# Performance work log

Measured on AMD Instinct MI355X. Metric: run time of the kernel, lower is better.

Reference implementation:

```python
import jax, jax.numpy as jnp
import numpy as np

N_DATA = 32768
N_CHK = 32768
N = N_DATA + N_CHK          # 65536 nodes
E = 524288                  # edges (before self-loops)
F_IN = 10                   # node_feature_dim
HID = 128                   # hidden_dim
HEADS = 4
C = HID // HEADS            # 32 per-head channels
L = 4                       # num_gnn_layers
EPS_LN = 1e-5


def layer_norm(x, g, b):
    mu = x.mean(-1, keepdims=True)
    var = ((x - mu) ** 2).mean(-1, keepdims=True)
    return (x - mu) * jax.lax.rsqrt(var + EPS_LN) * g + b


def mlp3(x, W1, b1, W2, b2, W3, b3):
    h = jax.nn.relu(x @ W1 + b1)
    h = jax.nn.relu(h @ W2 + b2)
    return h @ W3 + b3


def setup_inputs() -> dict:
    key = jax.random.key(0)
    ks = jax.random.split(key, 32)
    s = 0.02
    inp = {
        'node_features': jax.random.normal(ks[0], (N, F_IN), jnp.float32),
        'edge_index': jax.random.randint(ks[1], (2, E), 0, N, dtype=jnp.int64),
        # node embedding: Linear(F_IN,HID) + LayerNorm
        'W_emb': s * jax.random.normal(ks[2], (F_IN, HID), jnp.float32),
        'b_emb': jnp.zeros((HID,), jnp.float32),
        'ln0_g': jnp.ones((HID,), jnp.float32),
        'ln0_b': jnp.zeros((HID,), jnp.float32),
        # L GATConv layers (stacked): lin weight, att_src/att_dst, bias, post-LN
        'Wg': s * jax.random.normal(ks[3], (L, HID, HID), jnp.float32),
        'att_s': s * jax.random.normal(ks[4], (L, HEADS, C), jnp.float32),
        'att_d': s * jax.random.normal(ks[5], (L, HEADS, C), jnp.float32),
        'bg': jnp.zeros((L, HID), jnp.float32),
        'lng': jnp.ones((L, HID), jnp.float32),
        'lnb': jnp.zeros((L, HID), jnp.float32),
        # policy net
        'pW1': s * jax.random.normal(ks[6], (HID, HID), jnp.float32),
        'pb1': jnp.zeros((HID,), jnp.float32),
        'pW2': s * jax.random.normal(ks[7], (HID, HID // 2), jnp.float32),
        'pb2': jnp.zeros((HID // 2,), jnp.float32),
        'pW3': s * jax.random.normal(ks[8], (HID // 2, 2), jnp.float32),
        'pb3': jnp.zeros((2,), jnp.float32),
        # value net
        'vW1': s * jax.random.normal(ks[9], (HID, HID), jnp.float32),
        'vb1': jnp.zeros((HID,), jnp.float32),
        'vW2': s * jax.random.normal(ks[10], (HID, HID // 2), jnp.float32),
        'vb2': jnp.zeros((HID // 2,), jnp.float32),
        'vW3': s * jax.random.normal(ks[11], (HID // 2, 1), jnp.float32),
        'vb3': jnp.zeros((1,), jnp.float32),
    }
    return inp


def reference(node_features, edge_index, W_emb, b_emb, ln0_g, ln0_b,
              Wg, att_s, att_d, bg, lng, lnb,
              pW1, pb1, pW2, pb2, pW3, pb3,
              vW1, vb1, vW2, vb2, vW3, vb3):
    n = node_features.shape[0]
    # PyG GATConv adds self-loops by default
    loops = jnp.arange(n, dtype=edge_index.dtype)
    ei = jnp.concatenate([edge_index, jnp.stack([loops, loops])], axis=1)
    src, dst = ei[0], ei[1]

    # node embedding (dropout is identity in eval)
    x = jax.nn.relu(layer_norm(node_features @ W_emb + b_emb, ln0_g, ln0_b))

    for l in range(L):
        h = (x @ Wg[l]).reshape(n, HEADS, C)                       # [N,H,C]
        a_s = jnp.einsum('nhc,hc->nh', h, att_s[l])                # [N,H]
        a_d = jnp.einsum('nhc,hc->nh', h, att_d[l])
        alpha = jax.nn.leaky_relu(a_s[src] + a_d[dst], 0.2)        # [E+N,H]
        # segment softmax over destination node per head
        m = jax.ops.segment_max(alpha, dst, num_segments=n)
        alpha = jnp.exp(alpha - m[dst])
        denom = jax.ops.segment_sum(alpha, dst, num_segments=n)
        alpha = alpha / (denom[dst] + 1e-16)
        out = jax.ops.segment_sum(alpha[:, :, None] * h[src], dst,
                                  num_segments=n)                  # [N,H,C]
        out = out.reshape(n, HID) + bg[l]
        x = layer_norm(x + jax.nn.relu(out), lng[l], lnb[l])

    logits = mlp3(x[:N_DATA], pW1, pb1, pW2, pb2, pW3, pb3)        # [N_DATA,2]
    pooled = x.mean(axis=0, keepdims=True)                         # [1,HID]
    value = mlp3(pooled, vW1, vb1, vW2, vb2, vW3, vb3)             # [1,1]
    return logits, value
```

## Files before the change

kernel.cpp:

```cpp
#include <hip/hip_runtime.h>

#define NNODES 65536
#define NDATA  32768
#define HID    128
#define HEADS  4
#define CHANS  32
#define LAYERS 4

using bf16x8 = __attribute__((ext_vector_type(8))) short;
using f32x4  = __attribute__((ext_vector_type(4))) float;

__device__ __forceinline__ float wave_reduce_sum(float v) {
#pragma unroll
    for (int m = 1; m < 64; m <<= 1) v += __shfl_xor(v, m, 64);
    return v;
}

__device__ __forceinline__ unsigned short bf16_rne(float f) {
    unsigned u = __float_as_uint(f);
    return (unsigned short)((u + 0x7fffu + ((u >> 16) & 1u)) >> 16);
}
__device__ __forceinline__ float bf2f(unsigned short u) {
    return __uint_as_float((unsigned)u << 16);
}

__device__ __forceinline__ void gload_lds16(const unsigned short* g, unsigned short* l) {
    __builtin_amdgcn_global_load_lds(
        (const __attribute__((address_space(1))) void*)g,
        (__attribute__((address_space(3))) void*)l, 16, 0, 0);
}

__global__ void hist_kernel(const int* __restrict__ ei, int* __restrict__ deg, int Eo) {
    int e = blockIdx.x * 256 + threadIdx.x;
    if (e >= Eo) return;
    atomicAdd(&deg[ei[Eo + e]], 1);
}

__global__ void scan1(const int* __restrict__ deg, int* __restrict__ offs, int* __restrict__ bsum) {
    __shared__ int s[256];
    int t = threadIdx.x, b = blockIdx.x;
    int v = deg[b * 256 + t] + 1;
    s[t] = v;
    __syncthreads();
    for (int off = 1; off < 256; off <<= 1) {
        int add = (t >= off) ? s[t - off] : 0;
        __syncthreads();
        s[t] += add;
        __syncthreads();
    }
    offs[b * 256 + t] = s[t] - v;
    if (t == 255) bsum[b] = s[255];
}

__global__ void scan2(int* __restrict__ bsum) {
    __shared__ int s[256];
    int t = threadIdx.x;
    int v = bsum[t];
    s[t] = v;
    __syncthreads();
    for (int off = 1; off < 256; off <<= 1) {
        int add = (t >= off) ? s[t - off] : 0;
        __syncthreads();
        s[t] += add;
        __syncthreads();
    }
    bsum[t] = s[t] - v;
}

__global__ void scan3(int* __restrict__ offs, const int* __restrict__ bsum,
                      int* __restrict__ cursor, int Eo) {
    int i = blockIdx.x * 256 + threadIdx.x;
    int v = offs[i] + bsum[i >> 8];
    offs[i] = v;
    cursor[i] = v;
    if (i == 0) offs[NNODES] = Eo + NNODES;
}

__global__ void fill_kernel(const int* __restrict__ ei, int* __restrict__ cursor,
                            int* __restrict__ col, int Eo) {
    int e = blockIdx.x * 256 + threadIdx.x;
    int Etot = Eo + NNODES;
    if (e >= Etot) return;
    int src, dst;
    if (e < Eo) { src = ei[e]; dst = ei[Eo + e]; }
    else        { src = dst = e - Eo; }
    int pos = atomicAdd(&cursor[dst], 1);
    col[pos] = src;
}

__global__ void prep_wg(const float* __restrict__ Wg, const float* __restrict__ attS,
                        const float* __restrict__ attD,
                        unsigned short* __restrict__ wh, unsigned short* __restrict__ wl)
{
    int id = blockIdx.x * 256 + threadIdx.x;
    int l = id / (144 * 128);
    int rem = id % (144 * 128);
    int n = rem / 128, k = rem % 128;
    const float* W = Wg + (size_t)l * HID * HID;
    float v = 0.f;
    if (n < 128) {
        v = W[k * HID + n];
    } else if (n < 136) {
        int h = (n - 128) & 3;
        const float* av = ((n - 128) < 4 ? attS : attD) + l * HID + h * CHANS;
        for (int c = 0; c < CHANS; c++) v += W[k * HID + h * CHANS + c] * av[c];
    }
    unsigned short hh = bf16_rne(v);
    int t = n >> 4, bcol = n & 15;
    int ks = k >> 5, kq = (k >> 3) & 3, e = k & 7;
    size_t o = (size_t)l * (144 * 128) + (size_t)(((t * 4 + ks) * 64) + (kq * 16 + bcol)) * 8 + e;
    wh[o] = hh;
    wl[o] = bf16_rne(v - bf2f(hh));
}

__global__ void prep_heads(const float* __restrict__ pW1, const float* __restrict__ pW2,
                           const float* __restrict__ vW1, const float* __restrict__ vW2,
                           unsigned short* __restrict__ w1h, unsigned short* __restrict__ w1l,
                           unsigned short* __restrict__ w2h, unsigned short* __restrict__ w2l,
                           float* __restrict__ w1t, float* __restrict__ w2t)
{
    int id = blockIdx.x * 256 + threadIdx.x;
    if (id < 24576) {
        int n, k;
        float v;
        unsigned short *dh, *dl;
        if (id < 16384) {
            n = id / 128; k = id % 128;
            v = pW1[k * 128 + n];
            dh = w1h; dl = w1l;
        } else {
            int j = id - 16384;
            n = j / 128; k = j % 128;
            v = pW2[k * 64 + n];
            dh = w2h; dl = w2l;
        }
        unsigned short hh = bf16_rne(v);
        int t = n >> 4, bcol = n & 15;
        int ks = k >> 5, kq = (k >> 3) & 3, e = k & 7;
        size_t o = (size_t)(((t * 4 + ks) * 64) + (kq * 16 + bcol)) * 8 + e;
        dh[o] = hh;
        dl[o] = bf16_rne(v - bf2f(hh));
    } else {
        int j = id - 24576;
        if (j < 16384) {
            int t = j >> 7, k = j & 127;
            w1t[t * 128 + k] = vW1[k * 128 + t];
        } else {
            j -= 16384;
            int t = j >> 7, k = j & 127;
            w2t[t * 128 + k] = vW2[k * 64 + t];
        }
    }
}

__global__ __launch_bounds__(256) void embed_kernel(
    const float* __restrict__ feat, const float* __restrict__ W,
    const float* __restrict__ bb, const float* __restrict__ g,
    const float* __restrict__ be, unsigned short* __restrict__ xh,
    unsigned short* __restrict__ xl)
{
    int node = blockIdx.x * 4 + (threadIdx.x >> 6);
    int lane = threadIdx.x & 63;
    float f[10];
#pragma unroll
    for (int i = 0; i < 10; i++) f[i] = feat[node * 10 + i];
    int c0 = 2 * lane, c1 = c0 + 1;
    float v0 = bb[c0], v1 = bb[c1];
#pragma unroll
    for (int i = 0; i < 10; i++) {
        v0 = fmaf(f[i], W[i * HID + c0], v0);
        v1 = fmaf(f[i], W[i * HID + c1], v1);
    }
    float mu = wave_reduce_sum(v0 + v1) * (1.f / 128.f);
    float e0 = v0 - mu, e1 = v1 - mu;
    float var = wave_reduce_sum(e0 * e0 + e1 * e1) * (1.f / 128.f);
    float r = 1.f / sqrtf(var + 1e-5f);
    float r0 = fmaxf(e0 * r * g[c0] + be[c0], 0.f);
    float r1 = fmaxf(e1 * r * g[c1] + be[c1], 0.f);
    unsigned short h0 = bf16_rne(r0), h1 = bf16_rne(r1);
    unsigned short l0 = bf16_rne(r0 - bf2f(h0)), l1 = bf16_rne(r1 - bf2f(h1));
    size_t xi = (size_t)node * HID;
    *(unsigned*)(xh + xi + c0) = (unsigned)h0 | ((unsigned)h1 << 16);
    *(unsigned*)(xl + xi + c0) = (unsigned)l0 | ((unsigned)l1 << 16);
}

template <int NT, int EPI, bool ALO>
__global__ __launch_bounds__(512, 4) void mfma_gemm(
    const unsigned short* __restrict__ Ah, const unsigned short* __restrict__ Al,
    const unsigned short* __restrict__ Bh, const unsigned short* __restrict__ Bl,
    const float* __restrict__ bias,
    unsigned short* __restrict__ outH,
    float* __restrict__ a_s, float* __restrict__ a_d,
    const float* __restrict__ wfin, const float* __restrict__ bfin,
    float* __restrict__ outF)
{
    __shared__ unsigned short lds[NT * 2048];

    int tid = threadIdx.x;
    int wid = tid >> 6, l = tid & 63;
    int row = blockIdx.x * 128 + wid * 16 + (l & 15);
    int kg = (l >> 4) * 8;

    const unsigned short* arh = Ah + (size_t)row * 128 + kg;
    bf16x8 afh[4], afl[4];
#pragma unroll
    for (int ks = 0; ks < 4; ks++) afh[ks] = *(const bf16x8*)(arh + ks * 32);
    if constexpr (ALO) {
        const unsigned short* arl = Al + (size_t)row * 128 + kg;
#pragma unroll
        for (int ks = 0; ks < 4; ks++) afl[ks] = *(const bf16x8*)(arl + ks * 32);
    }

    f32x4 acc[NT];
#pragma unroll
    for (int t = 0; t < NT; t++) acc[t] = (f32x4){0.f, 0.f, 0.f, 0.f};

#pragma unroll
    for (int p = 0; p < 2; p++) {
        __syncthreads();
        for (int c = wid; c < 4 * NT; c += 8) {
            int fr = c >> 1, lo = c & 1;
            int t = fr >> 1, ksl = fr & 1;
            const unsigned short* src = (lo ? Bl : Bh)
                + ((size_t)(t * 4 + p * 2 + ksl) << 9) + ((unsigned)l << 3);
            gload_lds16(src, &lds[(size_t)c << 9]);
        }
        __syncthreads();
#pragma unroll
        for (int ksl = 0; ksl < 2; ksl++) {
            int ks = p * 2 + ksl;
#pragma unroll
            for (int t = 0; t < NT; t++) {
                const unsigned short* bp = &lds[(((t * 2 + ksl) << 1) << 9) + (l << 3)];
                bf16x8 bh  = *(const bf16x8*)bp;
                bf16x8 blo = *(const bf16x8*)(bp + 512);
                acc[t] = __builtin_amdgcn_mfma_f32_16x16x32_bf16(afh[ks], bh,  acc[t], 0, 0, 0);
                acc[t] = __builtin_amdgcn_mfma_f32_16x16x32_bf16(afh[ks], blo, acc[t], 0, 0, 0);
                if constexpr (ALO)
                    acc[t] = __builtin_amdgcn_mfma_f32_16x16x32_bf16(afl[ks], bh, acc[t], 0, 0, 0);
            }
        }
    }

    int ecol = l & 15;
    int er0 = blockIdx.x * 128 + wid * 16 + ((l >> 4) << 2);

    if constexpr (EPI == 0) {
#pragma unroll
        for (int t = 0; t < 8; t++)
#pragma unroll
            for (int j = 0; j < 4; j++)
                outH[(size_t)(er0 + j) * 128 + t * 16 + ecol] = bf16_rne(acc[t][j]);
#pragma unroll
        for (int j = 0; j < 4; j++) {
            float v = acc[8][j];
            if (ecol < 4)      a_s[(er0 + j) * 4 + ecol] = v;
            else if (ecol < 8) a_d[(er0 + j) * 4 + (ecol - 4)] = v;
        }
    } else if constexpr (EPI == 1) {
#pragma unroll
        for (int t = 0; t < NT; t++)
#pragma unroll
            for (int j = 0; j < 4; j++) {
                float v = fmaxf(acc[t][j] + bias[t * 16 + ecol], 0.f);
                outH[(size_t)(er0 + j) * 128 + t * 16 + ecol] = bf16_rne(v);
            }
    } else {
        float p0[4], p1[4];
#pragma unroll
        for (int j = 0; j < 4; j++) { p0[j] = 0.f; p1[j] = 0.f; }
#pragma unroll
        for (int t = 0; t < NT; t++) {
            int cc = t * 16 + ecol;
            float w0 = wfin[cc * 2 + 0], w1 = wfin[cc * 2 + 1];
#pragma unroll
            for (int j = 0; j < 4; j++) {
                float v = fmaxf(acc[t][j] + bias[cc], 0.f);
                p0[j] = fmaf(v, w0, p0[j]);
                p1[j] = fmaf(v, w1, p1[j]);
            }
        }
#pragma unroll
        for (int m = 1; m < 16; m <<= 1)
#pragma unroll
            for (int j = 0; j < 4; j++) {
                p0[j] += __shfl_xor(p0[j], m, 64);
                p1[j] += __shfl_xor(p1[j], m, 64);
            }
        if (ecol == 0) {
            float b0 = bfin[0], b1 = bfin[1];
#pragma unroll
            for (int j = 0; j < 4; j++) {
                outF[(er0 + j) * 2 + 0] = p0[j] + b0;
                outF[(er0 + j) * 2 + 1] = p1[j] + b1;
            }
        }
    }
}

__global__ __launch_bounds__(256) void gat_agg(
    const unsigned short* __restrict__ hb, const float* __restrict__ a_s,
    const float* __restrict__ a_d, const int* __restrict__ offs,
    const int* __restrict__ col, const float* __restrict__ bgl,
    const float* __restrict__ gl, const float* __restrict__ bl,
    unsigned short* __restrict__ xh, unsigned short* __restrict__ xl)
{
    __shared__ float wsm[4][64][4];
    __shared__ int   ssm[4][64];
    int wv = threadIdx.x >> 6;
    int lane = threadIdx.x & 63;
    int node = blockIdx.x * 4 + wv;
    int s = offs[node], e = offs[node + 1];
    int deg = e - s;
    float4 ad = *(const float4*)(a_d + (size_t)node * 4);

    int c0 = 2 * lane, c1 = 2 * lane + 1;
    int head = lane >> 4;
    float acc0 = 0.f, acc1 = 0.f;
    float den = 1e-16f;

    if (deg <= 64) {
        int src = 0;
        float4 wv4 = make_float4(0.f, 0.f, 0.f, 0.f);
        if (lane < deg) {
            src = col[s + lane];
            float4 as = *(const float4*)(a_s + (size_t)src * 4);
            float s0 = as.x + ad.x; s0 = (s0 > 0.f) ? s0 : 0.2f * s0;
            float s1 = as.y + ad.y; s1 = (s1 > 0.f) ? s1 : 0.2f * s1;
            float s2 = as.z + ad.z; s2 = (s2 > 0.f) ? s2 : 0.2f * s2;
            float s3 = as.w + ad.w; s3 = (s3 > 0.f) ? s3 : 0.2f * s3;
            wv4 = make_float4(expf(s0), expf(s1), expf(s2), expf(s3));
        }
        *(float4*)&wsm[wv][lane][0] = wv4;
        ssm[wv][lane] = src;
        int dg4 = (deg + 3) & ~3;
        for (int j = 0; j < dg4; j += 4) {
            int s0 = ssm[wv][j + 0], s1 = ssm[wv][j + 1];
            int s2 = ssm[wv][j + 2], s3 = ssm[wv][j + 3];
            float w0 = wsm[wv][j + 0][head], w1 = wsm[wv][j + 1][head];
            float w2 = wsm[wv][j + 2][head], w3 = wsm[wv][j + 3][head];
            unsigned v0 = *(const unsigned*)(hb + (((unsigned)s0 << 7) + (unsigned)c0));
            unsigned v1 = *(const unsigned*)(hb + (((unsigned)s1 << 7) + (unsigned)c0));
            unsigned v2 = *(const unsigned*)(hb + (((unsigned)s2 << 7) + (unsigned)c0));
            unsigned v3 = *(const unsigned*)(hb + (((unsigned)s3 << 7) + (unsigned)c0));
            den += (w0 + w1) + (w2 + w3);
            acc0 = fmaf(w0, __uint_as_float(v0 << 16), acc0);
            acc1 = fmaf(w0, __uint_as_float(v0 & 0xffff0000u), acc1);
            acc0 = fmaf(w1, __uint_as_float(v1 << 16), acc0);
            acc1 = fmaf(w1, __uint_as_float(v1 & 0xffff0000u), acc1);
            acc0 = fmaf(w2, __uint_as_float(v2 << 16), acc0);
            acc1 = fmaf(w2, __uint_as_float(v2 & 0xffff0000u), acc1);
            acc0 = fmaf(w3, __uint_as_float(v3 << 16), acc0);
            acc1 = fmaf(w3, __uint_as_float(v3 & 0xffff0000u), acc1);
        }
    } else {
        for (int j = s; j < e; j++) {
            int src = col[j];
            float4 as = *(const float4*)(a_s + (size_t)src * 4);
            float sh = (head == 0) ? (as.x + ad.x) : (head == 1) ? (as.y + ad.y)
                     : (head == 2) ? (as.z + ad.z) : (as.w + ad.w);
            sh = (sh > 0.f) ? sh : 0.2f * sh;
            float wj = expf(sh);
            den += wj;
            unsigned hv = *(const unsigned*)(hb + (((unsigned)src << 7) + (unsigned)c0));
            acc0 = fmaf(wj, __uint_as_float(hv << 16), acc0);
            acc1 = fmaf(wj, __uint_as_float(hv & 0xffff0000u), acc1);
        }
    }
    float inv = 1.f / den;
    acc0 *= inv;
    acc1 *= inv;

    float o0 = fmaxf(acc0 + bgl[c0], 0.f);
    float o1 = fmaxf(acc1 + bgl[c1], 0.f);
    size_t xi = (size_t)node * HID;
    unsigned ph = *(const unsigned*)(xh + xi + c0);
    unsigned pl = *(const unsigned*)(xl + xi + c0);
    float x0 = __uint_as_float(ph << 16) + __uint_as_float(pl << 16);
    float x1 = __uint_as_float(ph & 0xffff0000u) + __uint_as_float(pl & 0xffff0000u);
    float t0 = x0 + o0, t1 = x1 + o1;
    float mu = wave_reduce_sum(t0 + t1) * (1.f / 128.f);
    float e0 = t0 - mu, e1 = t1 - mu;
    float var = wave_reduce_sum(e0 * e0 + e1 * e1) * (1.f / 128.f);
    float r = 1.f / sqrtf(var + 1e-5f);
    float r0 = e0 * r * gl[c0] + bl[c0];
    float r1 = e1 * r * gl[c1] + bl[c1];
    unsigned short h0 = bf16_rne(r0), h1 = bf16_rne(r1);
    unsigned short l0 = bf16_rne(r0 - bf2f(h0)), l1 = bf16_rne(r1 - bf2f(h1));
    *(unsigned*)(xh + xi + c0) = (unsigned)h0 | ((unsigned)h1 << 16);
    *(unsigned*)(xl + xi + c0) = (unsigned)l0 | ((unsigned)l1 << 16);
}

__global__ void pool_sum(const unsigned short* __restrict__ xh,
                         const unsigned short* __restrict__ xl, float* __restrict__ partial) {
    int t = threadIdx.x;
    int base = blockIdx.x * 256;
    float s = 0.f;
    for (int i = 0; i < 256; i++) {
        size_t idx = (size_t)(base + i) * HID + t;
        s += bf2f(xh[idx]) + bf2f(xl[idx]);
    }
    partial[blockIdx.x * 128 + t] = s;
}

__global__ void value_mlp(const float* __restrict__ partial,
                          const float* __restrict__ w1t, const float* __restrict__ b1,
                          const float* __restrict__ w2t, const float* __restrict__ b2,
                          const float* __restrict__ W3, const float* __restrict__ b3,
                          float* __restrict__ out)
{
    __shared__ float p[128], h1[128], h2[64];
    int t = threadIdx.x;
    float s = 0.f;
    for (int i = 0; i < 256; i++) s += partial[i * 128 + t];
    p[t] = s * (1.f / (float)NNODES);
    __syncthreads();
    float a = b1[t];
    const float4* wr = (const float4*)(w1t + (size_t)t * 128);
#pragma unroll
    for (int k4 = 0; k4 < 32; k4++) {
        float4 w = wr[k4];
        a += p[4 * k4] * w.x + p[4 * k4 + 1] * w.y + p[4 * k4 + 2] * w.z + p[4 * k4 + 3] * w.w;
    }
    h1[t] = fmaxf(a, 0.f);
    __syncthreads();
    if (t < 64) {
        float a2 = b2[t];
        const float4* wr2 = (const float4*)(w2t + (size_t)t * 128);
#pragma unroll
        for (int k4 = 0; k4 < 32; k4++) {
            float4 w = wr2[k4];
            a2 += h1[4 * k4] * w.x + h1[4 * k4 + 1] * w.y + h1[4 * k4 + 2] * w.z + h1[4 * k4 + 3] * w.w;
        }
        h2[t] = fmaxf(a2, 0.f);
    }
    __syncthreads();
    if (t == 0) {
        float v = b3[0];
        for (int k = 0; k < 64; k++) v = fmaf(h2[k], W3[k], v);
        out[NDATA * 2] = v;
    }
}

extern "C" void kernel_launch(void* const* d_in, const int* in_sizes, int n_in,
                              void* d_out, int out_size, void* d_ws, size_t ws_size,
                              hipStream_t stream)
{
    const float* feat  = (const float*)d_in[0];
    const int*   ei    = (const int*)d_in[1];
    const float* W_emb = (const float*)d_in[2];
    const float* b_emb = (const float*)d_in[3];
    const float* ln0g  = (const float*)d_in[4];
    const float* ln0b  = (const float*)d_in[5];
    const float* Wg    = (const float*)d_in[6];
    const float* att_s = (const float*)d_in[7];
    const float* att_d = (const float*)d_in[8];
    const float* bg    = (const float*)d_in[9];
    const float* lng   = (const float*)d_in[10];
    const float* lnb   = (const float*)d_in[11];
    const float* pW1 = (const float*)d_in[12]; const float* pb1 = (const float*)d_in[13];
    const float* pW2 = (const float*)d_in[14]; const float* pb2 = (const float*)d_in[15];
    const float* pW3 = (const float*)d_in[16]; const float* pb3 = (const float*)d_in[17];
    const float* vW1 = (const float*)d_in[18]; const float* vb1 = (const float*)d_in[19];
    const float* vW2 = (const float*)d_in[20]; const float* vb2 = (const float*)d_in[21];
    const float* vW3 = (const float*)d_in[22]; const float* vb3 = (const float*)d_in[23];
    float* out = (float*)d_out;
    int Eo = in_sizes[1] / 2;

    unsigned short* xh = (unsigned short*)d_ws;
    unsigned short* xl = xh + (size_t)NNODES * HID;
    unsigned short* hb = xl + (size_t)NNODES * HID;
    float* a_s = (float*)(hb + (size_t)NNODES * HID);
    float* a_d = a_s + NNODES * HEADS;
    unsigned short* wgt_h = (unsigned short*)(a_d + NNODES * HEADS);
    unsigned short* wgt_l = wgt_h + 4 * 144 * 128;
    unsigned short* pw1h  = wgt_l + 4 * 144 * 128;
    unsigned short* pw1l  = pw1h + 128 * 128;
    unsigned short* pw2h  = pw1l + 128 * 128;
    unsigned short* pw2l  = pw2h + 64 * 128;
    float* w1t  = (float*)(pw2l + 64 * 128);
    float* w2t  = w1t + 128 * 128;
    float* partial = w2t + 64 * 128;
    int* deg    = (int*)(partial + 256 * 128);
    int* offs   = deg + NNODES;
    int* cursor = offs + NNODES + 2;
    int* bsum   = cursor + NNODES;
    int* col    = bsum + 256;
    unsigned short* ph1h = hb;

    prep_wg<<<4 * 144 * 128 / 256, 256, 0, stream>>>(Wg, att_s, att_d, wgt_h, wgt_l);
    prep_heads<<<192, 256, 0, stream>>>(pW1, pW2, vW1, vW2,
                                        pw1h, pw1l, pw2h, pw2l, w1t, w2t);

    hipMemsetAsync(deg, 0, (size_t)NNODES * 4, stream);
    hist_kernel<<<(Eo + 255) / 256, 256, 0, stream>>>(ei, deg, Eo);
    scan1<<<256, 256, 0, stream>>>(deg, offs, bsum);
    scan2<<<1, 256, 0, stream>>>(bsum);
    scan3<<<256, 256, 0, stream>>>(offs, bsum, cursor, Eo);
    fill_kernel<<<(Eo + NNODES + 255) / 256, 256, 0, stream>>>(ei, cursor, col, Eo);

    embed_kernel<<<NNODES / 4, 256, 0, stream>>>(feat, W_emb, b_emb, ln0g, ln0b, xh, xl);

    for (int l = 0; l < LAYERS; l++) {
        mfma_gemm<9, 0, true><<<NNODES / 128, 512, 0, stream>>>(
            xh, xl, wgt_h + (size_t)l * 144 * 128, wgt_l + (size_t)l * 144 * 128,
            nullptr, hb, a_s, a_d, nullptr, nullptr, nullptr);
        gat_agg<<<NNODES / 4, 256, 0, stream>>>(
            hb, a_s, a_d, offs, col, bg + l * HID, lng + l * HID, lnb + l * HID, xh, xl);
    }

    mfma_gemm<8, 1, true><<<NDATA / 128, 512, 0, stream>>>(
        xh, xl, pw1h, pw1l, pb1, ph1h, nullptr, nullptr, nullptr, nullptr, nullptr);
    mfma_gemm<4, 2, false><<<NDATA / 128, 512, 0, stream>>>(
        ph1h, nullptr, pw2h, pw2l, pb2, nullptr, nullptr, nullptr, pW3, pb3, out);

    pool_sum<<<256, 128, 0, stream>>>(xh, xl, partial);
    value_mlp<<<1, 128, 0, stream>>>(partial, w1t, vb1, w2t, vb2, vW3, vb3, out);
}
```

Before: 359.3 us.

## Drop activation low-part MFMA pass, use fast exp, merge prep kernels, pack LDS weights

Removes the activation low-bf16 correction term from the MFMA GEMMs, so each tile needs two MFMAs instead of three and the A low-part loads disappear. GAT aggregation now uses __expf and fmaxf-based leaky ReLU, and stores the weight and source index together as int2 rows per head in LDS. The two weight-prep kernels are merged into one launch. The price is lower GEMM precision, since the activation residual is ignored, plus a less accurate exp.

```diff
diff --git a/kernel.cpp b/kernel.cpp
--- a/kernel.cpp
+++ b/kernel.cpp
@@ -88,38 +88,38 @@
     col[pos] = src;
 }
 
-__global__ void prep_wg(const float* __restrict__ Wg, const float* __restrict__ attS,
-                        const float* __restrict__ attD,
-                        unsigned short* __restrict__ wh, unsigned short* __restrict__ wl)
+__global__ void prep_all(const float* __restrict__ Wg, const float* __restrict__ attS,
+                         const float* __restrict__ attD,
+                         const float* __restrict__ pW1, const float* __restrict__ pW2,
+                         const float* __restrict__ vW1, const float* __restrict__ vW2,
+                         unsigned short* __restrict__ wh, unsigned short* __restrict__ wl,
+                         unsigned short* __restrict__ w1h, unsigned short* __restrict__ w1l,
+                         unsigned short* __restrict__ w2h, unsigned short* __restrict__ w2l,
+                         float* __restrict__ w1t, float* __restrict__ w2t)
 {
     int id = blockIdx.x * 256 + threadIdx.x;
-    int l = id / (144 * 128);
-    int rem = id % (144 * 128);
-    int n = rem / 128, k = rem % 128;
-    const float* W = Wg + (size_t)l * HID * HID;
-    float v = 0.f;
-    if (n < 128) {
-        v = W[k * HID + n];
-    } else if (n < 136) {
-        int h = (n - 128) & 3;
-        const float* av = ((n - 128) < 4 ? attS : attD) + l * HID + h * CHANS;
-        for (int c = 0; c < CHANS; c++) v += W[k * HID + h * CHANS + c] * av[c];
-    }
-    unsigned short hh = bf16_rne(v);
-    int t = n >> 4, bcol = n & 15;
-    int ks = k >> 5, kq = (k >> 3) & 3, e = k & 7;
-    size_t o = (size_t)l * (144 * 128) + (size_t)(((t * 4 + ks) * 64) + (kq * 16 + bcol)) * 8 + e;
-    wh[o] = hh;
-    wl[o] = bf16_rne(v - bf2f(hh));
-}
-
-__global__ void prep_heads(const float* __restrict__ pW1, const float* __restrict__ pW2,
-                           const float* __restrict__ vW1, const float* __restrict__ vW2,
-                           unsigned short* __restrict__ w1h, unsigned short* __restrict__ w1l,
-                           unsigned short* __restrict__ w2h, unsigned short* __restrict__ w2l,
-                           float* __restrict__ w1t, float* __restrict__ w2t)
-{
-    int id = blockIdx.x * 256 + threadIdx.x;
+    if (id < 4 * 144 * 128) {
+        int l = id / (144 * 128);
+        int rem = id % (144 * 128);
+        int n = rem / 128, k = rem % 128;
+        const float* W = Wg + (size_t)l * HID * HID;
+        float v = 0.f;
+        if (n < 128) {
+            v = W[k * HID + n];
+        } else if (n < 136) {
+            int h = (n - 128) & 3;
+            const float* av = ((n - 128) < 4 ? attS : attD) + l * HID + h * CHANS;
+            for (int c = 0; c < CHANS; c++) v += W[k * HID + h * CHANS + c] * av[c];
+        }
+        unsigned short hh = bf16_rne(v);
+        int t = n >> 4, bcol = n & 15;
+        int ks = k >> 5, kq = (k >> 3) & 3, e = k & 7;
+        size_t o = (size_t)l * (144 * 128) + (size_t)(((t * 4 + ks) * 64) + (kq * 16 + bcol)) * 8 + e;
+        wh[o] = hh;
+        wl[o] = bf16_rne(v - bf2f(hh));
+        return;
+    }
+    id -= 4 * 144 * 128;
     if (id < 24576) {
         int n, k;
         float v;
@@ -140,16 +140,16 @@
         size_t o = (size_t)(((t * 4 + ks) * 64) + (kq * 16 + bcol)) * 8 + e;
         dh[o] = hh;
         dl[o] = bf16_rne(v - bf2f(hh));
-    } else {
-        int j = id - 24576;
-        if (j < 16384) {
-            int t = j >> 7, k = j & 127;
-            w1t[t * 128 + k] = vW1[k * 128 + t];
-        } else {
-            j -= 16384;
-            int t = j >> 7, k = j & 127;
-            w2t[t * 128 + k] = vW2[k * 64 + t];
-        }
+        return;
+    }
+    id -= 24576;
+    if (id < 16384) {
+        int t = id >> 7, k = id & 127;
+        w1t[t * 128 + k] = vW1[k * 128 + t];
+    } else if (id < 24576) {
+        int j = id - 16384;
+        int t = j >> 7, k = j & 127;
+        w2t[t * 128 + k] = vW2[k * 64 + t];
     }
 }
 
@@ -184,9 +184,9 @@
     *(unsigned*)(xl + xi + c0) = (unsigned)l0 | ((unsigned)l1 << 16);
 }
 
-template <int NT, int EPI, bool ALO>
+template <int NT, int EPI>
 __global__ __launch_bounds__(512, 4) void mfma_gemm(
-    const unsigned short* __restrict__ Ah, const unsigned short* __restrict__ Al,
+    const unsigned short* __restrict__ Ah,
     const unsigned short* __restrict__ Bh, const unsigned short* __restrict__ Bl,
     const float* __restrict__ bias,
     unsigned short* __restrict__ outH,
@@ -202,14 +202,9 @@
     int kg = (l >> 4) * 8;
 
     const unsigned short* arh = Ah + (size_t)row * 128 + kg;
-    bf16x8 afh[4], afl[4];
+    bf16x8 afh[4];
 #pragma unroll
     for (int ks = 0; ks < 4; ks++) afh[ks] = *(const bf16x8*)(arh + ks * 32);
-    if constexpr (ALO) {
-        const unsigned short* arl = Al + (size_t)row * 128 + kg;
-#pragma unroll
-        for (int ks = 0; ks < 4; ks++) afl[ks] = *(const bf16x8*)(arl + ks * 32);
-    }
 
     f32x4 acc[NT];
 #pragma unroll
@@ -236,8 +231,6 @@
                 bf16x8 blo = *(const bf16x8*)(bp + 512);
                 acc[t] = __builtin_amdgcn_mfma_f32_16x16x32_bf16(afh[ks], bh,  acc[t], 0, 0, 0);
                 acc[t] = __builtin_amdgcn_mfma_f32_16x16x32_bf16(afh[ks], blo, acc[t], 0, 0, 0);
-                if constexpr (ALO)
-                    acc[t] = __builtin_amdgcn_mfma_f32_16x16x32_bf16(afl[ks], bh, acc[t], 0, 0, 0);
             }
         }
     }
@@ -305,8 +298,7 @@
     const float* __restrict__ gl, const float* __restrict__ bl,
     unsigned short* __restrict__ xh, unsigned short* __restrict__ xl)
 {
-    __shared__ float wsm[4][64][4];
-    __shared__ int   ssm[4][64];
+    __shared__ int2 whs[4][4][64];
     int wv = threadIdx.x >> 6;
     int lane = threadIdx.x & 63;
     int node = blockIdx.x * 4 + wv;
@@ -321,28 +313,31 @@
 
     if (deg <= 64) {
         int src = 0;
-        float4 wv4 = make_float4(0.f, 0.f, 0.f, 0.f);
+        float e0 = 0.f, e1 = 0.f, e2 = 0.f, e3 = 0.f;
         if (lane < deg) {
             src = col[s + lane];
             float4 as = *(const float4*)(a_s + (size_t)src * 4);
-            float s0 = as.x + ad.x; s0 = (s0 > 0.f) ? s0 : 0.2f * s0;
-            float s1 = as.y + ad.y; s1 = (s1 > 0.f) ? s1 : 0.2f * s1;
-            float s2 = as.z + ad.z; s2 = (s2 > 0.f) ? s2 : 0.2f * s2;
-            float s3 = as.w + ad.w; s3 = (s3 > 0.f) ? s3 : 0.2f * s3;
-            wv4 = make_float4(expf(s0), expf(s1), expf(s2), expf(s3));
-        }
-        *(float4*)&wsm[wv][lane][0] = wv4;
-        ssm[wv][lane] = src;
+            float s0 = as.x + ad.x; s0 = fmaxf(s0, 0.2f * s0);
+            float s1 = as.y + ad.y; s1 = fmaxf(s1, 0.2f * s1);
+            float s2 = as.z + ad.z; s2 = fmaxf(s2, 0.2f * s2);
+            float s3 = as.w + ad.w; s3 = fmaxf(s3, 0.2f * s3);
+            e0 = __expf(s0); e1 = __expf(s1); e2 = __expf(s2); e3 = __expf(s3);
+        }
+        whs[wv][0][lane] = make_int2(__float_as_int(e0), src);
+        whs[wv][1][lane] = make_int2(__float_as_int(e1), src);
+        whs[wv][2][lane] = make_int2(__float_as_int(e2), src);
+        whs[wv][3][lane] = make_int2(__float_as_int(e3), src);
+        const int2* wrow = &whs[wv][head][0];
         int dg4 = (deg + 3) & ~3;
         for (int j = 0; j < dg4; j += 4) {
-            int s0 = ssm[wv][j + 0], s1 = ssm[wv][j + 1];
-            int s2 = ssm[wv][j + 2], s3 = ssm[wv][j + 3];
-            float w0 = wsm[wv][j + 0][head], w1 = wsm[wv][j + 1][head];
-            float w2 = wsm[wv][j + 2][head], w3 = wsm[wv][j + 3][head];
-            unsigned v0 = *(const unsigned*)(hb + (((unsigned)s0 << 7) + (unsigned)c0));
-            unsigned v1 = *(const unsigned*)(hb + (((unsigned)s1 << 7) + (unsigned)c0));
-            unsigned v2 = *(const unsigned*)(hb + (((unsigned)s2 << 7) + (unsigned)c0));
-            unsigned v3 = *(const unsigned*)(hb + (((unsigned)s3 << 7) + (unsigned)c0));
+            int2 q0 = wrow[j + 0], q1 = wrow[j + 1];
+            int2 q2 = wrow[j + 2], q3 = wrow[j + 3];
+            float w0 = __int_as_float(q0.x), w1 = __int_as_float(q1.x);
+            float w2 = __int_as_float(q2.x), w3 = __int_as_float(q3.x);
+            unsigned v0 = *(const unsigned*)(hb + (((unsigned)q0.y << 7) + (unsigned)c0));
+            unsigned v1 = *(const unsigned*)(hb + (((unsigned)q1.y << 7) + (unsigned)c0));
+            unsigned v2 = *(const unsigned*)(hb + (((unsigned)q2.y << 7) + (unsigned)c0));
+            unsigned v3 = *(const unsigned*)(hb + (((unsigned)q3.y << 7) + (unsigned)c0));
             den += (w0 + w1) + (w2 + w3);
             acc0 = fmaf(w0, __uint_as_float(v0 << 16), acc0);
             acc1 = fmaf(w0, __uint_as_float(v0 & 0xffff0000u), acc1);
@@ -359,8 +354,8 @@
             float4 as = *(const float4*)(a_s + (size_t)src * 4);
             float sh = (head == 0) ? (as.x + ad.x) : (head == 1) ? (as.y + ad.y)
                      : (head == 2) ? (as.z + ad.z) : (as.w + ad.w);
-            sh = (sh > 0.f) ? sh : 0.2f * sh;
-            float wj = expf(sh);
+            sh = fmaxf(sh, 0.2f * sh);
+            float wj = __expf(sh);
             den += wj;
             unsigned hv = *(const unsigned*)(hb + (((unsigned)src << 7) + (unsigned)c0));
             acc0 = fmaf(wj, __uint_as_float(hv << 16), acc0);
@@ -488,9 +483,9 @@
     int* col    = bsum + 256;
     unsigned short* ph1h = hb;
 
-    prep_wg<<<4 * 144 * 128 / 256, 256, 0, stream>>>(Wg, att_s, att_d, wgt_h, wgt_l);
-    prep_heads<<<192, 256, 0, stream>>>(pW1, pW2, vW1, vW2,
-                                        pw1h, pw1l, pw2h, pw2l, w1t, w2t);
+    prep_all<<<(4 * 144 * 128 + 24576 + 24576) / 256, 256, 0, stream>>>(
+        Wg, att_s, att_d, pW1, pW2, vW1, vW2,
+        wgt_h, wgt_l, pw1h, pw1l, pw2h, pw2l, w1t, w2t);
 
     hipMemsetAsync(deg, 0, (size_t)NNODES * 4, stream);
     hist_kernel<<<(Eo + 255) / 256, 256, 0, stream>>>(ei, deg, Eo);
@@ -502,17 +497,17 @@
     embed_kernel<<<NNODES / 4, 256, 0, stream>>>(feat, W_emb, b_emb, ln0g, ln0b, xh, xl);
 
     for (int l = 0; l < LAYERS; l++) {
-        mfma_gemm<9, 0, true><<<NNODES / 128, 512, 0, stream>>>(
-            xh, xl, wgt_h + (size_t)l * 144 * 128, wgt_l + (size_t)l * 144 * 128,
+        mfma_gemm<9, 0><<<NNODES / 128, 512, 0, stream>>>(
+            xh, wgt_h + (size_t)l * 144 * 128, wgt_l + (size_t)l * 144 * 128,
             nullptr, hb, a_s, a_d, nullptr, nullptr, nullptr);
         gat_agg<<<NNODES / 4, 256, 0, stream>>>(
             hb, a_s, a_d, offs, col, bg + l * HID, lng + l * HID, lnb + l * HID, xh, xl);
     }
 
-    mfma_gemm<8, 1, true><<<NDATA / 128, 512, 0, stream>>>(
-        xh, xl, pw1h, pw1l, pb1, ph1h, nullptr, nullptr, nullptr, nullptr, nullptr);
-    mfma_gemm<4, 2, false><<<NDATA / 128, 512, 0, stream>>>(
-        ph1h, nullptr, pw2h, pw2l, pb2, nullptr, nullptr, nullptr, pW3, pb3, out);
+    mfma_gemm<8, 1><<<NDATA / 128, 512, 0, stream>>>(
+        xh, pw1h, pw1l, pb1, ph1h, nullptr, nullptr, nullptr, nullptr, nullptr);
+    mfma_gemm<4, 2><<<NDATA / 128, 512, 0, stream>>>(
+        ph1h, pw2h, pw2l, pb2, nullptr, nullptr, nullptr, pW3, pb3, out);
 
     pool_sum<<<256, 128, 0, stream>>>(xh, xl, partial);
     value_mlp<<<1, 128, 0, stream>>>(partial, w1t, vb1, w2t, vb2, vW3, vb3, out);
```

New measurement: 348.6 us. 1.03x faster.
